# Kernel tuning notes

Measured on AMD Instinct MI355X. Metric: run time of the kernel, lower is better.

The kernel has to match this reference:

```python
import jax, jax.numpy as jnp
import numpy as np

B, N, E, C_IN, C_OUT = 4, 50000, 800000, 128, 128


def setup_inputs() -> dict:
    key = jax.random.key(0)
    k1, k2, k3, k4, k5 = jax.random.split(key, 5)
    x = jax.random.normal(k1, (B, N, C_IN), dtype=jnp.float32)
    edge_row = jax.random.randint(k2, (E,), 0, N, dtype=jnp.int32)
    edge_col = jax.random.randint(k3, (E,), 0, N, dtype=jnp.int32)
    edge_vals = jax.random.uniform(k4, (E,), dtype=jnp.float32)
    W = jax.random.normal(k5, (C_IN, C_OUT), dtype=jnp.float32) * 0.1  # weight_stddev=0.1
    b = jnp.full((C_OUT,), 0.1, dtype=jnp.float32)  # bias_constant=0.1
    return {"x": x, "edge_row": edge_row, "edge_col": edge_col,
            "edge_vals": edge_vals, "W": W, "b": b}


def reference(x, edge_row, edge_col, edge_vals, W, b):
    # Sparse adjacency aggregation: agg[b, r, :] = sum_e vals[e] * x[b, col[e], :]
    n = x.shape[1]

    def spmm(xb):  # xb: [N, C_in]
        msgs = xb[edge_col] * edge_vals[:, None]          # [E, C_in]
        return jax.ops.segment_sum(msgs, edge_row, num_segments=n)  # [N, C_in]

    agg = jax.vmap(spmm)(x)                               # [B, N, C_in]
    out = jnp.einsum('bnc,co->bno', agg, W) + b           # dense GEMM + bias
    return jax.nn.relu(out)
```

## Files before the change

### kernel.cpp

```cpp
#include <hip/hip_runtime.h>

#define NROWS 50000
#define BATCH 4
#define CH    128
#define CAP   64

typedef float  f32x4  __attribute__((ext_vector_type(4)));
typedef float  f32x2  __attribute__((ext_vector_type(2)));
typedef __bf16 bf16x8 __attribute__((ext_vector_type(8)));
typedef short  s16x8  __attribute__((ext_vector_type(8)));

static __device__ __forceinline__ unsigned short f2bf(float f) {
    unsigned u = __builtin_bit_cast(unsigned, f);
    u += 0x7fffu + ((u >> 16) & 1u);
    return (unsigned short)(u >> 16);
}

__global__ void k_scatter(const int* __restrict__ row, const int* __restrict__ col,
                          const float* __restrict__ vals, int E,
                          int* __restrict__ cnt, unsigned long long* __restrict__ csr) {
    int e = blockIdx.x * blockDim.x + threadIdx.x;
    if (e < E) {
        int r = row[e];
        int p = atomicAdd(&cnt[r], 1);
        if (p < CAP) {
            unsigned long long pk =
                (unsigned long long)(unsigned)col[e] |
                ((unsigned long long)__builtin_bit_cast(unsigned, vals[e]) << 32);
            csr[r * CAP + p] = pk;
        }
    }
}

__global__ __launch_bounds__(512, 4) void k_xw(const float* __restrict__ x,
                                               const float* __restrict__ W,
                                               unsigned short* __restrict__ y) {
    __shared__ unsigned short WtL[128 * 136];
    __shared__ unsigned short yt[8][16 * 136];
    const int tid = threadIdx.x;
    for (int idx = tid; idx < 128 * 128; idx += 512) {
        int k = idx >> 7, n = idx & 127;
        WtL[n * 136 + k] = f2bf(W[idx]);
    }
    __syncthreads();

    const int wave = tid >> 6;
    const int lane = tid & 63;
    const int m    = lane & 15;
    const int quad = lane >> 4;
    unsigned short* __restrict__ myt = yt[wave];

    const int NSTRIP = (BATCH * NROWS + 127) / 128;
    for (int s = blockIdx.x; s < NSTRIP; s += gridDim.x) {
        const int row0 = s * 128 + wave * 16;
        if (row0 >= BATCH * NROWS) continue;

        s16x8 a_s[4];
        const float* xr = x + (size_t)(row0 + m) * CH;
        #pragma unroll
        for (int kk = 0; kk < 4; ++kk) {
            const float4* p = (const float4*)(xr + kk * 32 + quad * 8);
            float4 f0 = p[0], f1 = p[1];
            s16x8 sv;
            sv[0] = f2bf(f0.x); sv[1] = f2bf(f0.y); sv[2] = f2bf(f0.z); sv[3] = f2bf(f0.w);
            sv[4] = f2bf(f1.x); sv[5] = f2bf(f1.y); sv[6] = f2bf(f1.z); sv[7] = f2bf(f1.w);
            a_s[kk] = sv;
        }

        #pragma unroll
        for (int nt = 0; nt < 8; ++nt) {
            f32x4 acc = {0.f, 0.f, 0.f, 0.f};
            #pragma unroll
            for (int kk = 0; kk < 4; ++kk) {
                bf16x8 b = *(const bf16x8*)&WtL[(nt * 16 + m) * 136 + kk * 32 + quad * 8];
                acc = __builtin_amdgcn_mfma_f32_16x16x32_bf16(
                          __builtin_bit_cast(bf16x8, a_s[kk]), b, acc, 0, 0, 0);
            }
            #pragma unroll
            for (int reg = 0; reg < 4; ++reg)
                myt[(quad * 4 + reg) * 136 + nt * 16 + m] = f2bf(acc[reg]);
        }

        #pragma unroll
        for (int it = 0; it < 4; ++it) {
            const int lrow = it * 4 + (lane >> 4);
            const int seg  = lane & 15;
            uint4 v = *(const uint4*)&myt[lrow * 136 + seg * 8];
            const int i  = row0 + lrow;
            const int bb = i / NROWS;
            const int n  = i - bb * NROWS;
            *(uint4*)&y[((size_t)n * BATCH + bb) * CH + seg * 8] = v;
        }
    }
}

__global__ __launch_bounds__(256) void k_spmm(const uint4* __restrict__ y4,
                                              const int* __restrict__ cnt,
                                              const unsigned long long* __restrict__ csr,
                                              const float* __restrict__ bias,
                                              float* __restrict__ out) {
    __shared__ unsigned long long lcsr[4][CAP];
    __shared__ float lout[4][4 * 132];
    const int tid  = threadIdx.x;
    const int wave = tid >> 6;
    const int lane = tid & 63;
    const int b    = lane >> 4;
    const int m    = lane & 15;
    const int r    = blockIdx.x * 4 + wave;
    const int deg  = min(cnt[r], CAP);
    if (lane < deg) lcsr[wave][lane] = csr[(size_t)r * CAP + lane];

    const uint4* __restrict__ Yl = y4 + lane;
    f32x2 acc[4];
    #pragma unroll
    for (int k = 0; k < 4; ++k) acc[k] = (f32x2){0.f, 0.f};

    int e = 0;
    for (; e + 8 <= deg; e += 8) {
        unsigned long long pk[8];
        #pragma unroll
        for (int j = 0; j < 8; ++j) pk[j] = lcsr[wave][e + j];
        uint4 u[8];
        #pragma unroll
        for (int j = 0; j < 8; ++j) u[j] = Yl[(size_t)(unsigned)pk[j] * 64];
        #pragma unroll
        for (int j = 0; j < 8; ++j) {
            float v = __builtin_bit_cast(float, (unsigned)(pk[j] >> 32));
            unsigned uu[4] = {u[j].x, u[j].y, u[j].z, u[j].w};
            #pragma unroll
            for (int k = 0; k < 4; ++k) {
                f32x2 p;
                p[0] = __builtin_bit_cast(float, uu[k] << 16);
                p[1] = __builtin_bit_cast(float, uu[k] & 0xffff0000u);
                acc[k] += v * p;
            }
        }
    }
    for (; e < deg; ++e) {
        unsigned long long pk = lcsr[wave][e];
        float v = __builtin_bit_cast(float, (unsigned)(pk >> 32));
        uint4 u = Yl[(size_t)(unsigned)pk * 64];
        unsigned uu[4] = {u.x, u.y, u.z, u.w};
        #pragma unroll
        for (int k = 0; k < 4; ++k) {
            f32x2 p;
            p[0] = __builtin_bit_cast(float, uu[k] << 16);
            p[1] = __builtin_bit_cast(float, uu[k] & 0xffff0000u);
            acc[k] += v * p;
        }
    }

    #pragma unroll
    for (int k = 0; k < 4; ++k) {
        float2 bv = ((const float2*)bias)[4 * m + k];
        float ox = fmaxf(acc[k][0] + bv.x, 0.f);
        float oy = fmaxf(acc[k][1] + bv.y, 0.f);
        *(float2*)&lout[wave][b * 132 + 8 * m + 2 * k] = make_float2(ox, oy);
    }
    __syncthreads();

    #pragma unroll
    for (int t = 0; t < 4; ++t) {
        unsigned long long pv = *(const unsigned long long*)&lout[t][wave * 132 + 2 * lane];
        unsigned long long* dst =
            (unsigned long long*)(out + ((size_t)wave * NROWS + blockIdx.x * 4 + t) * CH) + lane;
        __builtin_nontemporal_store(pv, dst);
    }
}

extern "C" void kernel_launch(void* const* d_in, const int* in_sizes, int n_in,
                              void* d_out, int out_size, void* d_ws, size_t ws_size,
                              hipStream_t stream) {
    const float* x        = (const float*)d_in[0];
    const int*   edge_row = (const int*)d_in[1];
    const int*   edge_col = (const int*)d_in[2];
    const float* edge_val = (const float*)d_in[3];
    const float* W        = (const float*)d_in[4];
    const float* bias     = (const float*)d_in[5];
    float*       out      = (float*)d_out;

    const int E = in_sizes[1];

    int*                cnt = (int*)d_ws;
    unsigned long long* csr = (unsigned long long*)(cnt + 50048);
    unsigned short*     y   = (unsigned short*)(csr + (size_t)NROWS * CAP);

    hipMemsetAsync(cnt, 0, 50048 * sizeof(int), stream);
    k_scatter<<<(E + 255) / 256, 256, 0, stream>>>(edge_row, edge_col, edge_val, E,
                                                   cnt, csr);
    k_xw<<<1563, 512, 0, stream>>>(x, W, y);
    k_spmm<<<NROWS / 4, 256, 0, stream>>>((const uint4*)y, cnt, csr, bias, out);
}
```

Measured before the change: 360.4 us.

## Process two rows per wave in SpMM with software-pipelined gathers and readlane indices

Each wave now handles two destination rows, interleaving their gather batches so loads for one row's next 8 edges are in flight while FMAs for the other run. Edge metadata is held in registers and broadcast with readlane instead of being staged through LDS. The block count is halved, and launch bounds now request 4 blocks per SM. The aim is more memory-level parallelism to hide gather latency, at the cost of doubled accumulator and load registers, which may reduce occupancy.

After: 362.5 us. About the same (+0.6%).

```diff
diff --git a/kernel.cpp b/kernel.cpp
--- a/kernel.cpp
+++ b/kernel.cpp
@@ -94,76 +94,93 @@
     }
 }
 
-__global__ __launch_bounds__(256) void k_spmm(const uint4* __restrict__ y4,
-                                              const int* __restrict__ cnt,
-                                              const unsigned long long* __restrict__ csr,
-                                              const float* __restrict__ bias,
-                                              float* __restrict__ out) {
-    __shared__ unsigned long long lcsr[4][CAP];
-    __shared__ float lout[4][4 * 132];
+static __device__ __forceinline__ void issue8(const uint4* __restrict__ Yl,
+                                              unsigned creg, unsigned vreg, int base,
+                                              uint4 (&u)[8], float (&sv)[8]) {
+    #pragma unroll
+    for (int j = 0; j < 8; ++j) {
+        unsigned cc = __builtin_amdgcn_readlane(creg, base + j);
+        sv[j] = __builtin_bit_cast(float, __builtin_amdgcn_readlane(vreg, base + j));
+        u[j] = Yl[(size_t)cc * 64];
+    }
+}
+static __device__ __forceinline__ void fma8(const uint4 (&u)[8], const float (&sv)[8],
+                                            f32x2 (&acc)[4]) {
+    #pragma unroll
+    for (int j = 0; j < 8; ++j) {
+        float v = sv[j];
+        unsigned uu[4] = {u[j].x, u[j].y, u[j].z, u[j].w};
+        #pragma unroll
+        for (int k = 0; k < 4; ++k) {
+            f32x2 p;
+            p[0] = __builtin_bit_cast(float, uu[k] << 16);
+            p[1] = __builtin_bit_cast(float, uu[k] & 0xffff0000u);
+            acc[k] += v * p;
+        }
+    }
+}
+
+__global__ __launch_bounds__(256, 4) void k_spmm(const uint4* __restrict__ y4,
+                                                 const int* __restrict__ cnt,
+                                                 const unsigned long long* __restrict__ csr,
+                                                 const float* __restrict__ bias,
+                                                 float* __restrict__ out) {
+    __shared__ float lout[8][4 * 132];
     const int tid  = threadIdx.x;
     const int wave = tid >> 6;
     const int lane = tid & 63;
     const int b    = lane >> 4;
     const int m    = lane & 15;
-    const int r    = blockIdx.x * 4 + wave;
-    const int deg  = min(cnt[r], CAP);
-    if (lane < deg) lcsr[wave][lane] = csr[(size_t)r * CAP + lane];
+    const int rA   = blockIdx.x * 8 + wave;
+    const int rB   = rA + 4;
+    const int degA = min(cnt[rA], CAP);
+    const int degB = min(cnt[rB], CAP);
+
+    unsigned long long pvA = csr[(size_t)rA * CAP + lane];
+    unsigned long long pvB = csr[(size_t)rB * CAP + lane];
+    if (lane >= degA) pvA = 0ull;
+    if (lane >= degB) pvB = 0ull;
+    const unsigned cA = (unsigned)pvA, vA = (unsigned)(pvA >> 32);
+    const unsigned cB = (unsigned)pvB, vB = (unsigned)(pvB >> 32);
 
     const uint4* __restrict__ Yl = y4 + lane;
-    f32x2 acc[4];
-    #pragma unroll
-    for (int k = 0; k < 4; ++k) acc[k] = (f32x2){0.f, 0.f};
-
-    int e = 0;
-    for (; e + 8 <= deg; e += 8) {
-        unsigned long long pk[8];
-        #pragma unroll
-        for (int j = 0; j < 8; ++j) pk[j] = lcsr[wave][e + j];
-        uint4 u[8];
-        #pragma unroll
-        for (int j = 0; j < 8; ++j) u[j] = Yl[(size_t)(unsigned)pk[j] * 64];
-        #pragma unroll
-        for (int j = 0; j < 8; ++j) {
-            float v = __builtin_bit_cast(float, (unsigned)(pk[j] >> 32));
-            unsigned uu[4] = {u[j].x, u[j].y, u[j].z, u[j].w};
-            #pragma unroll
-            for (int k = 0; k < 4; ++k) {
-                f32x2 p;
-                p[0] = __builtin_bit_cast(float, uu[k] << 16);
-                p[1] = __builtin_bit_cast(float, uu[k] & 0xffff0000u);
-                acc[k] += v * p;
-            }
-        }
-    }
-    for (; e < deg; ++e) {
-        unsigned long long pk = lcsr[wave][e];
-        float v = __builtin_bit_cast(float, (unsigned)(pk >> 32));
-        uint4 u = Yl[(size_t)(unsigned)pk * 64];
-        unsigned uu[4] = {u.x, u.y, u.z, u.w};
-        #pragma unroll
-        for (int k = 0; k < 4; ++k) {
-            f32x2 p;
-            p[0] = __builtin_bit_cast(float, uu[k] << 16);
-            p[1] = __builtin_bit_cast(float, uu[k] & 0xffff0000u);
-            acc[k] += v * p;
-        }
+    f32x2 accA[4], accB[4];
+    #pragma unroll
+    for (int k = 0; k < 4; ++k) { accA[k] = (f32x2){0.f, 0.f}; accB[k] = (f32x2){0.f, 0.f}; }
+
+    const int nA = (degA + 7) >> 3;
+    const int nB = (degB + 7) >> 3;
+    const int n  = nA > nB ? nA : nB;
+
+    uint4 uA[8], uB[8];
+    float svA[8], svB[8];
+    if (nA > 0) issue8(Yl, cA, vA, 0, uA, svA);
+    if (nB > 0) issue8(Yl, cB, vB, 0, uB, svB);
+
+    for (int it = 0; it < n; ++it) {
+        if (it < nA)     fma8(uA, svA, accA);
+        if (it + 1 < nA) issue8(Yl, cA, vA, (it + 1) * 8, uA, svA);
+        if (it < nB)     fma8(uB, svB, accB);
+        if (it + 1 < nB) issue8(Yl, cB, vB, (it + 1) * 8, uB, svB);
     }
 
     #pragma unroll
     for (int k = 0; k < 4; ++k) {
         float2 bv = ((const float2*)bias)[4 * m + k];
-        float ox = fmaxf(acc[k][0] + bv.x, 0.f);
-        float oy = fmaxf(acc[k][1] + bv.y, 0.f);
+        float ox = fmaxf(accA[k][0] + bv.x, 0.f);
+        float oy = fmaxf(accA[k][1] + bv.y, 0.f);
         *(float2*)&lout[wave][b * 132 + 8 * m + 2 * k] = make_float2(ox, oy);
+        ox = fmaxf(accB[k][0] + bv.x, 0.f);
+        oy = fmaxf(accB[k][1] + bv.y, 0.f);
+        *(float2*)&lout[wave + 4][b * 132 + 8 * m + 2 * k] = make_float2(ox, oy);
     }
     __syncthreads();
 
     #pragma unroll
-    for (int t = 0; t < 4; ++t) {
+    for (int t = 0; t < 8; ++t) {
         unsigned long long pv = *(const unsigned long long*)&lout[t][wave * 132 + 2 * lane];
         unsigned long long* dst =
-            (unsigned long long*)(out + ((size_t)wave * NROWS + blockIdx.x * 4 + t) * CH) + lane;
+            (unsigned long long*)(out + ((size_t)wave * NROWS + blockIdx.x * 8 + t) * CH) + lane;
         __builtin_nontemporal_store(pv, dst);
     }
 }
@@ -189,5 +206,5 @@
     k_scatter<<<(E + 255) / 256, 256, 0, stream>>>(edge_row, edge_col, edge_val, E,
                                                    cnt, csr);
     k_xw<<<1563, 512, 0, stream>>>(x, W, y);
-    k_spmm<<<NROWS / 4, 256, 0, stream>>>((const uint4*)y, cnt, csr, bias, out);
-}
+    k_spmm<<<NROWS / 8, 256, 0, stream>>>((const uint4*)y, cnt, csr, bias, out);
+}
```
